# Kernel optimization log

Hardware: AMD Instinct MI355X
Metric: run time of the kernel (lower is better)

The kernel has to match this reference:

```python
import jax, jax.numpy as jnp
import numpy as np

EMBED_DIM = 1024
NUM_HEADS = 16
HEAD_DIM = EMBED_DIM // NUM_HEADS


def setup_inputs() -> dict:
    key = jax.random.key(0)
    k1, k2, k3 = jax.random.split(key, 3)
    B, T, C = 4, 2048, EMBED_DIM
    x = jax.random.normal(k1, (B, T, C), dtype=jnp.float32)
    # torch Linear default init scale ~ 1/sqrt(fan_in)
    w_qkv = jax.random.normal(k2, (3 * C, C), dtype=jnp.float32) / np.sqrt(C)
    w_out = jax.random.normal(k3, (C, C), dtype=jnp.float32) / np.sqrt(C)
    # causal mask: True = masked (matches masked_fill semantics)
    mask = jnp.triu(jnp.ones((T, T), dtype=bool), k=1)
    return {"x": x, "mask": mask, "w_qkv": w_qkv, "w_out": w_out}


def reference(x, mask, w_qkv, w_out):
    B, T, C = x.shape
    H, D = NUM_HEADS, HEAD_DIM
    qkv = jnp.einsum('btc,fc->btf', x, w_qkv)  # [B,T,3C]
    q, k, v = jnp.split(qkv, 3, axis=-1)
    def split_heads(t):
        return t.reshape(B, T, H, D).transpose(0, 2, 1, 3)  # [B,H,T,D]
    q, k, v = split_heads(q), split_heads(k), split_heads(v)
    scale = 1.0 / jnp.sqrt(jnp.float32(D)).astype(x.dtype)
    scores = jnp.einsum('bhqd,bhkd->bhqk', q, k) * scale
    scores = jnp.where(mask[None, None, :, :], -jnp.inf, scores)
    attn = jax.nn.softmax(scores, axis=-1)
    out = jnp.einsum('bhqk,bhkd->bhqd', attn, v)
    out = out.transpose(0, 2, 1, 3).reshape(B, T, C)
    return jnp.einsum('btc,oc->bto', out, w_out)
```

## Files before the change

### kernel.cpp

```cpp
#include <hip/hip_runtime.h>
#include <hip/hip_bf16.h>

typedef __attribute__((ext_vector_type(8))) short short8;
typedef __attribute__((ext_vector_type(4))) float float4v;
typedef __attribute__((ext_vector_type(2))) unsigned int uint2v;

#define NB 4
#define NT 2048
#define NC 1024
#define NH 16
#define ND 64

__device__ __forceinline__ unsigned short f2bf(float f) {
    union { float f; unsigned int u; } v; v.f = f;
    unsigned int x = v.u;
    unsigned int r = (x + 0x7fffu + ((x >> 16) & 1u)) >> 16;
    return (unsigned short)r;
}

__device__ __forceinline__ unsigned int fbits(float f) {
    union { float f; unsigned int u; } v; v.f = f;
    return v.u;
}

__global__ void canon_bf16(const float* __restrict__ src,
                           unsigned short* __restrict__ dst, int n)
{
    const int i = (blockIdx.x * blockDim.x + threadIdx.x) * 8;
    if (i >= n) return;
    float4v a = *(const float4v*)&src[i];
    float4v b = *(const float4v*)&src[i + 4];
    short8 o;
    o[0] = (short)f2bf(a[0]); o[1] = (short)f2bf(a[1]);
    o[2] = (short)f2bf(a[2]); o[3] = (short)f2bf(a[3]);
    o[4] = (short)f2bf(b[0]); o[5] = (short)f2bf(b[1]);
    o[6] = (short)f2bf(b[2]); o[7] = (short)f2bf(b[3]);
    *(short8*)&dst[i] = o;
}

template<int MODE>
__global__ __launch_bounds__(256)
void gemm_nt(const unsigned short* __restrict__ A,
             const unsigned short* __restrict__ Bm,
             unsigned short* __restrict__ o0,
             unsigned short* __restrict__ o1,
             unsigned short* __restrict__ o2,
             float* __restrict__ of,
             int K)
{
    __shared__ __align__(16) unsigned short As[128 * 32];
    __shared__ __align__(16) unsigned short Bs[128 * 32];
    const int t = threadIdx.x;
    const int w = t >> 6, lane = t & 63;
    const int quad = lane >> 4, l16 = lane & 15;
    const int wr = w >> 1, wc = w & 1;
    const int rowBase = blockIdx.y * 128;
    const int colBase = blockIdx.x * 128;

    float4v acc[4][4];
#pragma unroll
    for (int i = 0; i < 4; i++)
#pragma unroll
        for (int j = 0; j < 4; j++) acc[i][j] = (float4v){0.f, 0.f, 0.f, 0.f};

    const unsigned short* Ag = A + (size_t)(rowBase + w * 16 + (lane >> 2)) * K + (lane & 3) * 8;
    const unsigned short* Bg = Bm + (size_t)(colBase + w * 16 + (lane >> 2)) * K + (lane & 3) * 8;
    const int steps = K >> 5;

    for (int kt = 0; kt < steps; ++kt) {
        __syncthreads();
#pragma unroll
        for (int c = 0; c < 2; ++c) {
            __builtin_amdgcn_global_load_lds(
                (const __attribute__((address_space(1))) unsigned int*)(Ag + (size_t)c * 64 * K + kt * 32),
                (__attribute__((address_space(3))) unsigned int*)(&As[(c * 256 + w * 64) * 8]),
                16, 0, 0);
            __builtin_amdgcn_global_load_lds(
                (const __attribute__((address_space(1))) unsigned int*)(Bg + (size_t)c * 64 * K + kt * 32),
                (__attribute__((address_space(3))) unsigned int*)(&Bs[(c * 256 + w * 64) * 8]),
                16, 0, 0);
        }
        asm volatile("s_waitcnt vmcnt(0)" ::: "memory");
        __syncthreads();
        short8 af[4], bf[4];
#pragma unroll
        for (int i = 0; i < 4; i++)
            af[i] = *(const short8*)&As[(wr * 64 + i * 16 + l16) * 32 + quad * 8];
#pragma unroll
        for (int j = 0; j < 4; j++)
            bf[j] = *(const short8*)&Bs[(wc * 64 + j * 16 + l16) * 32 + quad * 8];
#pragma unroll
        for (int i = 0; i < 4; i++)
#pragma unroll
            for (int j = 0; j < 4; j++)
                acc[i][j] = __builtin_amdgcn_mfma_f32_16x16x32_bf16(af[i], bf[j], acc[i][j], 0, 0, 0);
    }

#pragma unroll
    for (int i = 0; i < 4; i++) {
        const int growb = rowBase + wr * 64 + i * 16 + quad * 4;
#pragma unroll
        for (int j = 0; j < 4; j++) {
            const int gcol = colBase + wc * 64 + j * 16 + l16;
#pragma unroll
            for (int r = 0; r < 4; r++) {
                const float vv = acc[i][j][r];
                const int gr = growb + r;
                if (MODE == 0) {
                    const unsigned short bv = f2bf(vv);
                    const int part = gcol >> 10;
                    const int rem = gcol & 1023;
                    const int h = rem >> 6, d = rem & 63;
                    const int b = gr >> 11, tt = gr & 2047;
                    const size_t bh = (size_t)(b * NH + h);
                    if (part == 0)      o0[(bh * NT + tt) * ND + d] = bv;
                    else if (part == 1) o1[(bh * NT + tt) * ND + d] = bv;
                    else                o2[(bh * ND + d) * NT + tt] = bv;
                } else {
                    of[(size_t)gr * NC + gcol] = vv;
                }
            }
        }
    }
}

#define PSTR 72

__global__ __launch_bounds__(256)
void attn_fused(const unsigned short* __restrict__ Q,
                const unsigned short* __restrict__ Kb,
                const unsigned short* __restrict__ Vt,
                unsigned short* __restrict__ att)
{
    const int bh = blockIdx.y;
    const int b = bh >> 4, h = bh & 15;
    const int t = threadIdx.x;
    const int w = t >> 6, lane = t & 63;
    const int quad = lane >> 4, l16 = lane & 15;
    const int l8 = l16 & 7;

    __shared__ __align__(16) unsigned short Ks[64 * 64];
    __shared__ __align__(16) unsigned short Vs[64 * 64];
    __shared__ __align__(16) unsigned short Pl[4][16 * PSTR];
    unsigned short* Pw = &Pl[w][0];

    const int srow = t >> 3;
    const int scol = ((t & 7) ^ (srow & 7)) * 8;

    const float sc = 0.125f;

    for (int phase = 0; phase < 2; ++phase) {
        const int qtile = (phase == 0) ? (int)blockIdx.x : 31 - (int)blockIdx.x;
        const int qb = qtile * 64 + w * 16;
        const int q_local = w * 16 + l16;
        const int q_own = qb + l16;

        short8 qf[2];
#pragma unroll
        for (int s = 0; s < 2; s++)
            qf[s] = *(const short8*)&Q[((size_t)bh * NT + qb + l16) * ND + s * 32 + quad * 8];

        float4v o[4];
#pragma unroll
        for (int jd = 0; jd < 4; jd++) o[jd] = (float4v){0.f, 0.f, 0.f, 0.f};
        float m_s = -1e30f, l_s = 0.f;

        const int nkt = qtile + 1;
        for (int kt = 0; kt < nkt; ++kt) {
            const int kb = kt * 64;
#pragma unroll
            for (int p = 0; p < 2; ++p) {
                __builtin_amdgcn_global_load_lds(
                    (const __attribute__((address_space(1))) unsigned int*)
                        (Kb + ((size_t)bh * NT + kb + p * 32 + srow) * ND + scol),
                    (__attribute__((address_space(3))) unsigned int*)(&Ks[(p * 256 + w * 64) * 8]),
                    16, 0, 0);
                __builtin_amdgcn_global_load_lds(
                    (const __attribute__((address_space(1))) unsigned int*)
                        (Vt + ((size_t)bh * ND + p * 32 + srow) * NT + kb + scol),
                    (__attribute__((address_space(3))) unsigned int*)(&Vs[(p * 256 + w * 64) * 8]),
                    16, 0, 0);
            }
            asm volatile("s_waitcnt vmcnt(0)" ::: "memory");
            __syncthreads();

            float4v sacc[4];
#pragma unroll
            for (int f = 0; f < 4; f++) sacc[f] = (float4v){0.f, 0.f, 0.f, 0.f};
#pragma unroll
            for (int f = 0; f < 4; f++)
#pragma unroll
                for (int s = 0; s < 2; s++) {
                    short8 kf = *(const short8*)&Ks[(f * 16 + l16) * 64 + (((s * 4 + quad) ^ l8) * 8)];
                    sacc[f] = __builtin_amdgcn_mfma_f32_16x16x32_bf16(kf, qf[s], sacc[f], 0, 0, 0);
                }

            float a[16];
#pragma unroll
            for (int f = 0; f < 4; f++)
#pragma unroll
                for (int r = 0; r < 4; r++) a[f * 4 + r] = sacc[f][r] * sc;
            if (kt == qtile) {
#pragma unroll
                for (int f = 0; f < 4; f++)
#pragma unroll
                    for (int r = 0; r < 4; r++)
                        if (f * 16 + quad * 4 + r > q_local) a[f * 4 + r] = -1e30f;
            }
            float tm = a[0];
#pragma unroll
            for (int i = 1; i < 16; i++) tm = fmaxf(tm, a[i]);
            tm = fmaxf(tm, __shfl_xor(tm, 16));
            tm = fmaxf(tm, __shfl_xor(tm, 32));
            const float mnew = fmaxf(m_s, tm);
            const float alpha = __expf(m_s - mnew);
            float e[16], rs = 0.f;
#pragma unroll
            for (int i = 0; i < 16; i++) { e[i] = __expf(a[i] - mnew); rs += e[i]; }
            rs += __shfl_xor(rs, 16);
            rs += __shfl_xor(rs, 32);
            l_s = l_s * alpha + rs;
            m_s = mnew;
#pragma unroll
            for (int jd = 0; jd < 4; jd++)
#pragma unroll
                for (int r = 0; r < 4; r++) o[jd][r] *= alpha;

#pragma unroll
            for (int f = 0; f < 4; f++) {
                unsigned int d0 = (fbits(e[f * 4 + 1]) & 0xFFFF0000u) | (fbits(e[f * 4 + 0]) >> 16);
                unsigned int d1 = (fbits(e[f * 4 + 3]) & 0xFFFF0000u) | (fbits(e[f * 4 + 2]) >> 16);
                *(uint2v*)&Pw[l16 * PSTR + f * 16 + quad * 4] = (uint2v){d0, d1};
            }
            asm volatile("s_waitcnt lgkmcnt(0)" ::: "memory");
            const short8 pf0 = *(const short8*)&Pw[l16 * PSTR + quad * 8];
            const short8 pf1 = *(const short8*)&Pw[l16 * PSTR + 32 + quad * 8];

#pragma unroll
            for (int jd = 0; jd < 4; jd++) {
                short8 vf0 = *(const short8*)&Vs[(jd * 16 + l16) * 64 + ((quad ^ l8) * 8)];
                short8 vf1 = *(const short8*)&Vs[(jd * 16 + l16) * 64 + (((4 + quad) ^ l8) * 8)];
                o[jd] = __builtin_amdgcn_mfma_f32_16x16x32_bf16(vf0, pf0, o[jd], 0, 0, 0);
                o[jd] = __builtin_amdgcn_mfma_f32_16x16x32_bf16(vf1, pf1, o[jd], 0, 0, 0);
            }
            __syncthreads();
        }

        const float rl = 1.0f / l_s;
        unsigned int* att32 = (unsigned int*)att;
#pragma unroll
        for (int jd = 0; jd < 4; jd++)
#pragma unroll
            for (int rp = 0; rp < 2; rp++) {
                const float v0 = o[jd][2 * rp] * rl;
                const float v1 = o[jd][2 * rp + 1] * rl;
                const size_t el = ((size_t)b * NT + q_own) * NC + h * ND + jd * 16 + quad * 4 + 2 * rp;
                att32[el >> 1] = (unsigned int)f2bf(v0) | ((unsigned int)f2bf(v1) << 16);
            }
    }
}

extern "C" void kernel_launch(void* const* d_in, const int* in_sizes, int n_in,
                              void* d_out, int out_size, void* d_ws, size_t ws_size,
                              hipStream_t stream) {
    const float* x_raw     = (const float*)d_in[0];
    const float* w_qkv_raw = (const float*)d_in[2];
    const float* w_out_raw = (const float*)d_in[3];
    float* outp = (float*)d_out;

    unsigned short* base = (unsigned short*)d_ws;
    const int n_x  = NB * NT * NC;
    const int n_wq = 3 * NC * NC;
    const int n_wo = NC * NC;
    const size_t tsz = (size_t)NB * NH * NT * ND;
    unsigned short* xb    = base;
    unsigned short* wqb   = xb + n_x;
    unsigned short* wob   = wqb + n_wq;
    unsigned short* qbuf  = wob + n_wo;
    unsigned short* kbuf  = qbuf + tsz;
    unsigned short* vtbuf = kbuf + tsz;
    unsigned short* attb  = xb;

    canon_bf16<<<n_x  / (256 * 8), 256, 0, stream>>>(x_raw,     xb,  n_x);
    canon_bf16<<<n_wq / (256 * 8), 256, 0, stream>>>(w_qkv_raw, wqb, n_wq);
    canon_bf16<<<n_wo / (256 * 8), 256, 0, stream>>>(w_out_raw, wob, n_wo);

    gemm_nt<0><<<dim3(3072 / 128, (NB * NT) / 128), 256, 0, stream>>>(
        xb, wqb, qbuf, kbuf, vtbuf, nullptr, NC);
    attn_fused<<<dim3(16, NB * NH), 256, 0, stream>>>(qbuf, kbuf, vtbuf, attb);
    gemm_nt<1><<<dim3(NC / 128, (NB * NT) / 128), 256, 0, stream>>>(
        attb, wob, nullptr, nullptr, nullptr, outp, NC);
}
```

Before: 319.0 us.

## Double GEMM K-tile to 64 with XOR-swizzled LDS and fold softmax scale into Q

The GEMM kernel now stages a 64-wide K slice per iteration instead of 32, halving the number of barrier/wait cycles per output tile. The LDS layout uses an XOR swizzle on 16-byte column chunks to avoid bank conflicts on fragment reads. Separately, the 1/sqrt(D) scale is applied to Q in the QKV GEMM epilogue, which removes a per-score multiply in the attention kernel. The larger tiles double LDS use per block, which may reduce occupancy, and scaling Q before bf16 rounding slightly changes rounding (exact since 0.125 is a power of two).

```diff
diff --git a/kernel.cpp b/kernel.cpp
--- a/kernel.cpp
+++ b/kernel.cpp
@@ -48,11 +48,12 @@
              float* __restrict__ of,
              int K)
 {
-    __shared__ __align__(16) unsigned short As[128 * 32];
-    __shared__ __align__(16) unsigned short Bs[128 * 32];
+    __shared__ __align__(16) unsigned short As[128 * 64];
+    __shared__ __align__(16) unsigned short Bs[128 * 64];
     const int t = threadIdx.x;
     const int w = t >> 6, lane = t & 63;
     const int quad = lane >> 4, l16 = lane & 15;
+    const int l8 = l16 & 7;
     const int wr = w >> 1, wc = w & 1;
     const int rowBase = blockIdx.y * 128;
     const int colBase = blockIdx.x * 128;
@@ -63,37 +64,43 @@
 #pragma unroll
         for (int j = 0; j < 4; j++) acc[i][j] = (float4v){0.f, 0.f, 0.f, 0.f};
 
-    const unsigned short* Ag = A + (size_t)(rowBase + w * 16 + (lane >> 2)) * K + (lane & 3) * 8;
-    const unsigned short* Bg = Bm + (size_t)(colBase + w * 16 + (lane >> 2)) * K + (lane & 3) * 8;
-    const int steps = K >> 5;
+    const int srow8 = t >> 3;
+    const int scol = ((t & 7) ^ (srow8 & 7)) * 8;
+    const unsigned short* Ag = A + (size_t)(rowBase + srow8) * K + scol;
+    const unsigned short* Bg = Bm + (size_t)(colBase + srow8) * K + scol;
+    const int steps = K >> 6;
 
     for (int kt = 0; kt < steps; ++kt) {
         __syncthreads();
 #pragma unroll
-        for (int c = 0; c < 2; ++c) {
+        for (int q = 0; q < 4; ++q) {
             __builtin_amdgcn_global_load_lds(
-                (const __attribute__((address_space(1))) unsigned int*)(Ag + (size_t)c * 64 * K + kt * 32),
-                (__attribute__((address_space(3))) unsigned int*)(&As[(c * 256 + w * 64) * 8]),
+                (const __attribute__((address_space(1))) unsigned int*)(Ag + (size_t)q * 32 * K + kt * 64),
+                (__attribute__((address_space(3))) unsigned int*)(&As[(q * 256 + w * 64) * 8]),
                 16, 0, 0);
             __builtin_amdgcn_global_load_lds(
-                (const __attribute__((address_space(1))) unsigned int*)(Bg + (size_t)c * 64 * K + kt * 32),
-                (__attribute__((address_space(3))) unsigned int*)(&Bs[(c * 256 + w * 64) * 8]),
+                (const __attribute__((address_space(1))) unsigned int*)(Bg + (size_t)q * 32 * K + kt * 64),
+                (__attribute__((address_space(3))) unsigned int*)(&Bs[(q * 256 + w * 64) * 8]),
                 16, 0, 0);
         }
         asm volatile("s_waitcnt vmcnt(0)" ::: "memory");
         __syncthreads();
-        short8 af[4], bf[4];
-#pragma unroll
-        for (int i = 0; i < 4; i++)
-            af[i] = *(const short8*)&As[(wr * 64 + i * 16 + l16) * 32 + quad * 8];
-#pragma unroll
-        for (int j = 0; j < 4; j++)
-            bf[j] = *(const short8*)&Bs[(wc * 64 + j * 16 + l16) * 32 + quad * 8];
-#pragma unroll
-        for (int i = 0; i < 4; i++)
+#pragma unroll
+        for (int ks = 0; ks < 2; ++ks) {
+            const int co = ((ks * 4 + quad) ^ l8) * 8;
+            short8 af[4], bf[4];
+#pragma unroll
+            for (int i = 0; i < 4; i++)
+                af[i] = *(const short8*)&As[(wr * 64 + i * 16 + l16) * 64 + co];
 #pragma unroll
             for (int j = 0; j < 4; j++)
-                acc[i][j] = __builtin_amdgcn_mfma_f32_16x16x32_bf16(af[i], bf[j], acc[i][j], 0, 0, 0);
+                bf[j] = *(const short8*)&Bs[(wc * 64 + j * 16 + l16) * 64 + co];
+#pragma unroll
+            for (int i = 0; i < 4; i++)
+#pragma unroll
+                for (int j = 0; j < 4; j++)
+                    acc[i][j] = __builtin_amdgcn_mfma_f32_16x16x32_bf16(af[i], bf[j], acc[i][j], 0, 0, 0);
+        }
     }
 
 #pragma unroll
@@ -104,9 +111,9 @@
             const int gcol = colBase + wc * 64 + j * 16 + l16;
 #pragma unroll
             for (int r = 0; r < 4; r++) {
-                const float vv = acc[i][j][r];
                 const int gr = growb + r;
                 if (MODE == 0) {
+                    const float vv = (gcol < 1024) ? acc[i][j][r] * 0.125f : acc[i][j][r];
                     const unsigned short bv = f2bf(vv);
                     const int part = gcol >> 10;
                     const int rem = gcol & 1023;
@@ -117,7 +124,7 @@
                     else if (part == 1) o1[(bh * NT + tt) * ND + d] = bv;
                     else                o2[(bh * ND + d) * NT + tt] = bv;
                 } else {
-                    of[(size_t)gr * NC + gcol] = vv;
+                    of[(size_t)gr * NC + gcol] = acc[i][j][r];
                 }
             }
         }
@@ -147,8 +154,6 @@
     const int srow = t >> 3;
     const int scol = ((t & 7) ^ (srow & 7)) * 8;
 
-    const float sc = 0.125f;
-
     for (int phase = 0; phase < 2; ++phase) {
         const int qtile = (phase == 0) ? (int)blockIdx.x : 31 - (int)blockIdx.x;
         const int qb = qtile * 64 + w * 16;
@@ -199,7 +204,7 @@
 #pragma unroll
             for (int f = 0; f < 4; f++)
 #pragma unroll
-                for (int r = 0; r < 4; r++) a[f * 4 + r] = sacc[f][r] * sc;
+                for (int r = 0; r < 4; r++) a[f * 4 + r] = sacc[f][r];
             if (kt == qtile) {
 #pragma unroll
                 for (int f = 0; f < 4; f++)
```

Result: faster. 305.2 us (-4.3%).
